# Kernel optimization log

Hardware: AMD Instinct MI355X
Metric: run time of the kernel (lower is better)

## Reference

```python
import jax, jax.numpy as jnp
import numpy as np

B, L, H = 2, 2048, 1024
NH, KVH = 16, 4
HD = H // NH          # 64
G = NH // KVH         # 4 query heads per kv head


def setup_inputs() -> dict:
    key = jax.random.key(0)
    ks = jax.random.split(key, 10)
    s = 0.02
    return {
        "hidden_states": jax.random.normal(ks[0], (B, L, H), dtype=jnp.float32),
        "attention_mask": jnp.zeros((B, 1, L, L), dtype=jnp.float32),
        "Wq": jax.random.normal(ks[1], (H, H), dtype=jnp.float32) * s,
        "bq": jnp.zeros((H,), dtype=jnp.float32),
        "Wk": jax.random.normal(ks[2], (KVH * HD, H), dtype=jnp.float32) * s,
        "bk": jnp.zeros((KVH * HD,), dtype=jnp.float32),
        "Wv": jax.random.normal(ks[3], (KVH * HD, H), dtype=jnp.float32) * s,
        "bv": jnp.zeros((KVH * HD,), dtype=jnp.float32),
        "Wo": jax.random.normal(ks[4], (H, H), dtype=jnp.float32) * s,
        "bo": jnp.zeros((H,), dtype=jnp.float32),
    }


def reference(hidden_states, attention_mask, Wq, bq, Wk, bk, Wv, bv, Wo, bo):
    x = hidden_states
    # projections (torch Linear: x @ W.T + b)
    q = (x @ Wq.T + bq).reshape(B, L, NH, HD).transpose(0, 2, 1, 3)   # [B,NH,L,HD]
    k = (x @ Wk.T + bk).reshape(B, L, KVH, HD).transpose(0, 2, 1, 3)  # [B,KVH,L,HD]
    v = (x @ Wv.T + bv).reshape(B, L, KVH, HD).transpose(0, 2, 1, 3)
    # GQA: group query heads per kv head instead of repeat_interleave (same math)
    qg = q.reshape(B, KVH, G, L, HD)
    scores = jnp.einsum("bkgqd,bkld->bkgql", qg, k) / jnp.sqrt(jnp.float32(HD))
    scores = scores + attention_mask[:, :, None, :, :]  # mask broadcasts over heads
    attn = jax.nn.softmax(scores, axis=-1)              # dropout p=0 -> identity
    ctx = jnp.einsum("bkgql,bkld->bkgqd", attn, v)      # [B,KVH,G,L,HD]
    ctx = ctx.reshape(B, NH, L, HD).transpose(0, 2, 1, 3).reshape(B, L, H)
    return ctx @ Wo.T + bo
```

## Files before the change

kernel.cpp:

```cpp
#include <hip/hip_runtime.h>

#define B_   2
#define L_   2048
#define H_   1024
#define NH_  16
#define KVH_ 4
#define HD_  64

typedef short short8 __attribute__((ext_vector_type(8)));
typedef float f32x4 __attribute__((ext_vector_type(4)));
typedef unsigned short u16x4 __attribute__((ext_vector_type(4)));
typedef unsigned int u32x2 __attribute__((ext_vector_type(2)));

#define LOG2E 1.4426950408889634f
#define QSC   0.18033688011112042f
#define MFMA  __builtin_amdgcn_mfma_f32_16x16x32_bf16

#if __has_builtin(__builtin_amdgcn_exp2f)
#define EXP2(x) __builtin_amdgcn_exp2f(x)
#else
#define EXP2(x) exp2f(x)
#endif

static __device__ __forceinline__ unsigned short f2bf(float f) {
  unsigned int u = __float_as_uint(f);
  u += 0x7FFFu + ((u >> 16) & 1u);
  return (unsigned short)(u >> 16);
}

static __device__ __forceinline__ unsigned int cvtpk(float lo, float hi) {
  unsigned int r;
  asm("v_cvt_pk_bf16_f32 %0, %1, %2" : "=v"(r) : "v"(lo), "v"(hi));
  return r;
}

static __device__ __forceinline__ void gload_lds16(const void* g, void* l) {
  __builtin_amdgcn_global_load_lds(
      (const __attribute__((address_space(1))) unsigned int*)g,
      (__attribute__((address_space(3))) unsigned int*)l, 16, 0, 0);
}

__global__ __launch_bounds__(256) void k_prep(const float* __restrict__ x,
                                              const float* __restrict__ Wq,
                                              const float* __restrict__ Wk,
                                              const float* __restrict__ Wv,
                                              const float* __restrict__ Wo,
                                              const float* __restrict__ mask,
                                              unsigned short* __restrict__ xb,
                                              unsigned short* __restrict__ wcat,
                                              unsigned short* __restrict__ wo_b,
                                              unsigned char* __restrict__ flags) {
  const int blk = blockIdx.x;
  const int t = threadIdx.x;
  if (blk < 4096) {
    size_t i = ((size_t)blk * 256 + t) * 4;
    float4 v = *(const float4*)(x + i);
    u16x4 o = { f2bf(v.x), f2bf(v.y), f2bf(v.z), f2bf(v.w) };
    *(u16x4*)(xb + i) = o;
  } else if (blk < 6656) {
    int r = blk - 4096;
    int c = t * 4;
    const float* src;
    unsigned short* dst;
    if (r < 1024)      { src = Wq + (size_t)r * 1024;          dst = wcat + (size_t)r * 1024; }
    else if (r < 1280) { src = Wk + (size_t)(r - 1024) * 1024; dst = wcat + (size_t)r * 1024; }
    else if (r < 1536) { src = Wv + (size_t)(r - 1280) * 1024; dst = wcat + (size_t)r * 1024; }
    else               { src = Wo + (size_t)(r - 1536) * 1024; dst = wo_b + (size_t)(r - 1536) * 1024; }
    float4 v = *(const float4*)(src + c);
    u16x4 o = { f2bf(v.x), f2bf(v.y), f2bf(v.z), f2bf(v.w) };
    *(u16x4*)(dst + c) = o;
  } else {
    const int mb = blk - 6656;
    const int b = mb >> 10, qb = (mb >> 5) & 31, kb = mb & 31;
    const float* base = mask + ((size_t)b * L_ + qb * 64) * L_ + kb * 64;
    const int r0 = t >> 4, c = (t & 15) * 4;
    bool nz = false;
#pragma unroll
    for (int i = 0; i < 4; ++i) {
      float4 v = *(const float4*)(base + (size_t)(r0 + i * 16) * L_ + c);
      nz |= (v.x != 0.f) | (v.y != 0.f) | (v.z != 0.f) | (v.w != 0.f);
    }
    __shared__ int anyv;
    if (t == 0) anyv = 0;
    __syncthreads();
    if (__any(nz) && (t & 63) == 0) atomicOr(&anyv, 1);
    __syncthreads();
    if (t == 0) flags[mb] = (unsigned char)anyv;
  }
}

template <int MODE>
__global__ __launch_bounds__(256) void k_gemm(const unsigned short* __restrict__ A,
                                              const unsigned short* __restrict__ Bt,
                                              const float* __restrict__ bias0,
                                              const float* __restrict__ bias1,
                                              const float* __restrict__ bias2,
                                              unsigned short* __restrict__ q_ws,
                                              unsigned short* __restrict__ k_ws,
                                              unsigned short* __restrict__ vt_ws,
                                              float* __restrict__ outp) {
  const int bn = blockIdx.x, bm = blockIdx.y;
  const int t = threadIdx.x;
  const int lane = t & 63, li = lane & 15, g = lane >> 4;
  const int wid = t >> 6, wr = wid >> 1, wc = wid & 1;
  __shared__ unsigned short lds_a[128 * 32];
  __shared__ unsigned short lds_b[128 * 32];

  const f32x4 z = {0.f, 0.f, 0.f, 0.f};
  f32x4 acc[4][4];
#pragma unroll
  for (int m = 0; m < 4; ++m)
#pragma unroll
    for (int n = 0; n < 4; ++n) acc[m][n] = z;

  const int c0 = t, c1 = 256 + t;
  const int r0 = c0 >> 2, o0 = (c0 & 3) * 8;
  const int r1 = c1 >> 2, o1 = (c1 & 3) * 8;
  const unsigned short* a0p = A + (size_t)(bm * 128 + r0) * 1024 + o0;
  const unsigned short* a1p = A + (size_t)(bm * 128 + r1) * 1024 + o1;
  const unsigned short* b0p = Bt + (size_t)(bn * 128 + r0) * 1024 + o0;
  const unsigned short* b1p = Bt + (size_t)(bn * 128 + r1) * 1024 + o1;

  for (int kt = 0; kt < 1024; kt += 32) {
    gload_lds16(a0p + kt, &lds_a[c0 * 8]);
    gload_lds16(a1p + kt, &lds_a[c1 * 8]);
    gload_lds16(b0p + kt, &lds_b[c0 * 8]);
    gload_lds16(b1p + kt, &lds_b[c1 * 8]);
    __syncthreads();
    short8 af[4], bf[4];
#pragma unroll
    for (int m = 0; m < 4; ++m) af[m] = *(const short8*)&lds_a[(wr * 64 + m * 16 + li) * 32 + g * 8];
#pragma unroll
    for (int n = 0; n < 4; ++n) bf[n] = *(const short8*)&lds_b[(wc * 64 + n * 16 + li) * 32 + g * 8];
#pragma unroll
    for (int m = 0; m < 4; ++m)
#pragma unroll
      for (int n = 0; n < 4; ++n)
        acc[m][n] = MFMA(af[m], bf[n], acc[m][n], 0, 0, 0);
    __syncthreads();
  }

#pragma unroll
  for (int m = 0; m < 4; ++m) {
    const int row0 = bm * 128 + wr * 64 + m * 16 + 4 * g;
#pragma unroll
    for (int n = 0; n < 4; ++n) {
      const int col = bn * 128 + wc * 64 + n * 16 + li;
      f32x4 v = acc[m][n];
      if (MODE == 1) {
        const float bias = bias0[col];
#pragma unroll
        for (int r = 0; r < 4; ++r) outp[(size_t)(row0 + r) * 1024 + col] = v[r] + bias;
      } else {
        if (col < 1024) {
          const float bias = bias0[col];
#pragma unroll
          for (int r = 0; r < 4; ++r) q_ws[(size_t)(row0 + r) * 1024 + col] = f2bf((v[r] + bias) * QSC);
        } else if (col < 1280) {
          const int cc = col - 1024;
          const float bias = bias1[cc];
#pragma unroll
          for (int r = 0; r < 4; ++r) k_ws[(size_t)(row0 + r) * 256 + cc] = f2bf(v[r] + bias);
        } else {
          const int cc = col - 1280;
          const float bias = bias2[cc];
          const int kvh = cc >> 6, d = cc & 63;
          const int b = row0 >> 11, l0 = row0 & 2047;
          u16x4 pk = { f2bf(v[0] + bias), f2bf(v[1] + bias), f2bf(v[2] + bias), f2bf(v[3] + bias) };
          *(u16x4*)(vt_ws + ((size_t)((b * KVH_ + kvh) * 64 + d)) * 2048 + l0) = pk;
        }
      }
    }
  }
}

__global__ __launch_bounds__(256, 2) void k_attn(const unsigned short* __restrict__ q_ws,
                                                 const unsigned short* __restrict__ k_ws,
                                                 const unsigned short* __restrict__ vt_ws,
                                                 const float* __restrict__ mask,
                                                 const unsigned char* __restrict__ mflags,
                                                 unsigned short* __restrict__ ctx) {
  const int bk = blockIdx.x;
  const int qt = blockIdx.y;
  const int b = bk >> 2, kvh = bk & 3;
  const int t = threadIdx.x;
  const int wid = t >> 6, lane = t & 63, li = lane & 15, g = lane >> 4;
  const int h = kvh * 4 + wid;

  __shared__ unsigned short lds_k[3][64 * 64];
  __shared__ unsigned short lds_v[3][64 * 64];
  __shared__ unsigned short lds_p[4][2][16 * 72];

  const unsigned short* qlane = q_ws + ((size_t)b * L_ + qt * 32 + li) * H_ + h * HD_ + g * 8;
  short8 qf[2][2];
#pragma unroll
  for (int qif = 0; qif < 2; ++qif)
#pragma unroll
    for (int hh = 0; hh < 2; ++hh)
      qf[qif][hh] = *(const short8*)(qlane + (size_t)qif * 16 * H_ + hh * 32);

  const unsigned int* fp = (const unsigned int*)(mflags + b * 1024 + (qt >> 1) * 32);
  unsigned int fm = 0;
#pragma unroll
  for (int w = 0; w < 8; ++w) {
    unsigned int wv = fp[w];
    fm |= ((wv & 0x000000FFu) ? 1u : 0u) << (w * 4 + 0);
    fm |= ((wv & 0x0000FF00u) ? 1u : 0u) << (w * 4 + 1);
    fm |= ((wv & 0x00FF0000u) ? 1u : 0u) << (w * 4 + 2);
    fm |= ((wv & 0xFF000000u) ? 1u : 0u) << (w * 4 + 3);
  }
  fm = __builtin_amdgcn_readfirstlane(fm);

  const int srow = t >> 3, sgr = t & 7;
  const int swz = (sgr ^ (srow & 7)) * 8;
  const unsigned short* ksrc = k_ws + ((size_t)b * L_ + srow) * 256 + kvh * 64 + swz;
  const unsigned short* vsrc = vt_ws + ((size_t)(b * KVH_ + kvh) * 64 + srow) * 2048 + swz;

  const f32x4 z = {0.f, 0.f, 0.f, 0.f};
  f32x4 o[2][4];
#pragma unroll
  for (int qif = 0; qif < 2; ++qif)
#pragma unroll
    for (int db = 0; db < 4; ++db) o[qif][db] = z;
  float l_run[2] = {0.f, 0.f};

  const int rsw = li & 7;

#define STAGE(buf, kt)                                                       \
  {                                                                          \
    _Pragma("unroll")                                                        \
    for (int i = 0; i < 2; ++i) {                                            \
      gload_lds16(ksrc + ((size_t)(kt) * 64 + i * 32) * 256,                 \
                  &lds_k[buf][(t + 256 * i) * 8]);                           \
      gload_lds16(vsrc + (size_t)i * 32 * 2048 + (kt) * 64,                  \
                  &lds_v[buf][(t + 256 * i) * 8]);                           \
    }                                                                        \
  }

  auto readK = [&](short8 (&kf)[4][2], int buf) {
#pragma unroll
    for (int x = 0; x < 4; ++x) {
      const int row = (x * 16 + li) * 64;
      kf[x][0] = *(const short8*)&lds_k[buf][row + ((0 + g) ^ rsw) * 8];
      kf[x][1] = *(const short8*)&lds_k[buf][row + ((4 + g) ^ rsw) * 8];
    }
  };

  auto tile = [&](short8 (&kfc)[4][2], short8 (&kfn)[4][2], int kt) {
    const int cur = kt % 3;
    if (kt + 2 < 32) STAGE((kt + 2) % 3, kt + 2);

    short8 vf[4][2];
#pragma unroll
    for (int x = 0; x < 4; ++x) {
      const int row = (x * 16 + li) * 64;
      vf[x][0] = *(const short8*)&lds_v[cur][row + ((0 + g) ^ rsw) * 8];
      vf[x][1] = *(const short8*)&lds_v[cur][row + ((4 + g) ^ rsw) * 8];
    }

    f32x4 sv[2][4];
    __builtin_amdgcn_s_setprio(1);
#pragma unroll
    for (int qif = 0; qif < 2; ++qif)
#pragma unroll
      for (int kb = 0; kb < 4; ++kb) {
        sv[qif][kb] = MFMA(kfc[kb][0], qf[qif][0], z, 0, 0, 0);
        sv[qif][kb] = MFMA(kfc[kb][1], qf[qif][1], sv[qif][kb], 0, 0, 0);
      }
    __builtin_amdgcn_s_setprio(0);

    if (kt + 1 < 32) readK(kfn, (kt + 1) % 3);

    if (fm & (1u << kt)) {
#pragma unroll
      for (int qif = 0; qif < 2; ++qif) {
        const float* mrow = mask + ((size_t)b * L_ + qt * 32 + qif * 16 + li) * L_ + kt * 64 + 4 * g;
#pragma unroll
        for (int kb = 0; kb < 4; ++kb) {
          float4 mv = *(const float4*)(mrow + kb * 16);
          sv[qif][kb][0] = fmaf(mv.x, LOG2E, sv[qif][kb][0]);
          sv[qif][kb][1] = fmaf(mv.y, LOG2E, sv[qif][kb][1]);
          sv[qif][kb][2] = fmaf(mv.z, LOG2E, sv[qif][kb][2]);
          sv[qif][kb][3] = fmaf(mv.w, LOG2E, sv[qif][kb][3]);
        }
      }
    }

#pragma unroll
    for (int qif = 0; qif < 2; ++qif) {
      float ts = 0.f;
#pragma unroll
      for (int kb = 0; kb < 4; ++kb)
#pragma unroll
        for (int r = 0; r < 4; ++r) {
          const float p = EXP2(sv[qif][kb][r]);
          sv[qif][kb][r] = p;
          ts += p;
        }
      l_run[qif] += ts;
#pragma unroll
      for (int kb = 0; kb < 4; ++kb) {
        u32x2 pk = { cvtpk(sv[qif][kb][0], sv[qif][kb][1]),
                     cvtpk(sv[qif][kb][2], sv[qif][kb][3]) };
        *(u32x2*)&lds_p[wid][qif][li * 72 + kb * 16 + 4 * g] = pk;
      }
    }

    __builtin_amdgcn_s_setprio(1);
#pragma unroll
    for (int qif = 0; qif < 2; ++qif)
#pragma unroll
      for (int kjh = 0; kjh < 2; ++kjh) {
        short8 pb = *(const short8*)&lds_p[wid][qif][li * 72 + kjh * 32 + g * 8];
#pragma unroll
        for (int db = 0; db < 4; ++db)
          o[qif][db] = MFMA(vf[db][kjh], pb, o[qif][db], 0, 0, 0);
      }
    __builtin_amdgcn_s_setprio(0);

    __syncthreads();
  };

  STAGE(0, 0);
  __syncthreads();
  STAGE(1, 1);
  __syncthreads();

  short8 kfA[4][2], kfB[4][2];
  readK(kfA, 0);

#pragma unroll 1
  for (int kt = 0; kt < 32; kt += 2) {
    tile(kfA, kfB, kt);
    tile(kfB, kfA, kt + 1);
  }
#undef STAGE

#pragma unroll
  for (int qif = 0; qif < 2; ++qif) {
    float lt = l_run[qif];
    lt += __shfl_xor(lt, 16);
    lt += __shfl_xor(lt, 32);
    const float inv = 1.0f / lt;
    unsigned short* cp = ctx + ((size_t)b * L_ + qt * 32 + qif * 16 + li) * H_ + h * HD_ + 4 * g;
#pragma unroll
    for (int db = 0; db < 4; ++db) {
      u32x2 pk = { cvtpk(o[qif][db][0] * inv, o[qif][db][1] * inv),
                   cvtpk(o[qif][db][2] * inv, o[qif][db][3] * inv) };
      *(u32x2*)(cp + db * 16) = pk;
    }
  }
}

extern "C" void kernel_launch(void* const* d_in, const int* in_sizes, int n_in,
                              void* d_out, int out_size, void* d_ws, size_t ws_size,
                              hipStream_t stream) {
  const float* x    = (const float*)d_in[0];
  const float* mask = (const float*)d_in[1];
  const float* Wq   = (const float*)d_in[2];
  const float* bq   = (const float*)d_in[3];
  const float* Wk   = (const float*)d_in[4];
  const float* bk   = (const float*)d_in[5];
  const float* Wv   = (const float*)d_in[6];
  const float* bv   = (const float*)d_in[7];
  const float* Wo   = (const float*)d_in[8];
  const float* bo   = (const float*)d_in[9];
  float* out = (float*)d_out;

  char* ws = (char*)d_ws;
  unsigned short* xb    = (unsigned short*)(ws);
  unsigned short* ctx   = xb;
  unsigned short* wcat  = (unsigned short*)(ws + 8388608);
  unsigned short* wo_b  = (unsigned short*)(ws + 11534336);
  unsigned short* q_ws  = (unsigned short*)(ws + 13631488);
  unsigned short* k_ws  = (unsigned short*)(ws + 22020096);
  unsigned short* vt_ws = (unsigned short*)(ws + 24117248);
  unsigned char*  mflg  = (unsigned char*)(ws + 26214400);

  k_prep<<<dim3(8704), dim3(256), 0, stream>>>(x, Wq, Wk, Wv, Wo, mask, xb, wcat, wo_b, mflg);
  k_gemm<0><<<dim3(12, 32), dim3(256), 0, stream>>>(xb, wcat, bq, bk, bv, q_ws, k_ws, vt_ws, nullptr);
  k_attn<<<dim3(8, 64), dim3(256), 0, stream>>>(q_ws, k_ws, vt_ws, mask, mflg, ctx);
  k_gemm<1><<<dim3(8, 32), dim3(256), 0, stream>>>(ctx, wo_b, bo, nullptr, nullptr,
                                                   nullptr, nullptr, nullptr, out);
}
```

Measured before the change: 116.5 us.

## Restructure attention with 32x32 MFMA, register P via permlane swap, split-K waves

The attention kernel switches from 16x16x32 to 32x32x16 bf16 MFMA. Each wave now handles two query heads over half of the key tile, with partial outputs and row sums combined through LDS at the end. The probability tile is moved into the PV operand layout with v_permlane32_swap instead of an LDS round trip, and K/V staging drops from triple to double buffering. The aim is to cut LDS traffic and instruction count per tile, at the cost of a final cross-wave reduction and less prefetch depth.

```diff
diff --git a/kernel.cpp b/kernel.cpp
--- a/kernel.cpp
+++ b/kernel.cpp
@@ -9,12 +9,13 @@
 
 typedef short short8 __attribute__((ext_vector_type(8)));
 typedef float f32x4 __attribute__((ext_vector_type(4)));
+typedef float f32x16 __attribute__((ext_vector_type(16)));
 typedef unsigned short u16x4 __attribute__((ext_vector_type(4)));
-typedef unsigned int u32x2 __attribute__((ext_vector_type(2)));
 
 #define LOG2E 1.4426950408889634f
 #define QSC   0.18033688011112042f
-#define MFMA  __builtin_amdgcn_mfma_f32_16x16x32_bf16
+#define MFMA   __builtin_amdgcn_mfma_f32_16x16x32_bf16
+#define MFMA32 __builtin_amdgcn_mfma_f32_32x32x16_bf16
 
 #if __has_builtin(__builtin_amdgcn_exp2f)
 #define EXP2(x) __builtin_amdgcn_exp2f(x)
@@ -32,6 +33,17 @@
   unsigned int r;
   asm("v_cvt_pk_bf16_f32 %0, %1, %2" : "=v"(r) : "v"(lo), "v"(hi));
   return r;
+}
+
+static __device__ __forceinline__ void plswap(unsigned int& a, unsigned int& b) {
+  asm("v_permlane32_swap_b32 %0, %1" : "+v"(a), "+v"(b));
+}
+
+static __device__ __forceinline__ short8 mk8(unsigned int w0, unsigned int w1,
+                                             unsigned int w2, unsigned int w3) {
+  union { unsigned int u[4]; short8 s; } x;
+  x.u[0] = w0; x.u[1] = w1; x.u[2] = w2; x.u[3] = w3;
+  return x.s;
 }
 
 static __device__ __forceinline__ void gload_lds16(const void* g, void* l) {
@@ -184,20 +196,21 @@
   const int qt = blockIdx.y;
   const int b = bk >> 2, kvh = bk & 3;
   const int t = threadIdx.x;
-  const int wid = t >> 6, lane = t & 63, li = lane & 15, g = lane >> 4;
-  const int h = kvh * 4 + wid;
-
-  __shared__ unsigned short lds_k[3][64 * 64];
-  __shared__ unsigned short lds_v[3][64 * 64];
-  __shared__ unsigned short lds_p[4][2][16 * 72];
-
-  const unsigned short* qlane = q_ws + ((size_t)b * L_ + qt * 32 + li) * H_ + h * HD_ + g * 8;
-  short8 qf[2][2];
-#pragma unroll
-  for (int qif = 0; qif < 2; ++qif)
-#pragma unroll
-    for (int hh = 0; hh < 2; ++hh)
-      qf[qif][hh] = *(const short8*)(qlane + (size_t)qif * 16 * H_ + hh * 32);
+  const int wid = t >> 6, lane = t & 63;
+  const int l31 = lane & 31, g1 = lane >> 5;
+  const int kh = wid >> 1, hp = wid & 1;
+
+  __shared__ unsigned short smem[16384];
+  __shared__ float lred[2][2][64];
+
+  const unsigned short* qbase = q_ws + ((size_t)b * L_ + qt * 32 + l31) * H_ +
+                                (kvh * 4 + hp * 2) * 64 + g1 * 8;
+  short8 qf[2][4];
+#pragma unroll
+  for (int h2 = 0; h2 < 2; ++h2)
+#pragma unroll
+    for (int ks = 0; ks < 4; ++ks)
+      qf[h2][ks] = *(const short8*)(qbase + h2 * 64 + ks * 16);
 
   const unsigned int* fp = (const unsigned int*)(mflags + b * 1024 + (qt >> 1) * 32);
   unsigned int fm = 0;
@@ -216,138 +229,178 @@
   const unsigned short* ksrc = k_ws + ((size_t)b * L_ + srow) * 256 + kvh * 64 + swz;
   const unsigned short* vsrc = vt_ws + ((size_t)(b * KVH_ + kvh) * 64 + srow) * 2048 + swz;
 
-  const f32x4 z = {0.f, 0.f, 0.f, 0.f};
-  f32x4 o[2][4];
-#pragma unroll
-  for (int qif = 0; qif < 2; ++qif)
-#pragma unroll
-    for (int db = 0; db < 4; ++db) o[qif][db] = z;
-  float l_run[2] = {0.f, 0.f};
-
-  const int rsw = li & 7;
-
-#define STAGE(buf, kt)                                                       \
-  {                                                                          \
-    _Pragma("unroll")                                                        \
-    for (int i = 0; i < 2; ++i) {                                            \
-      gload_lds16(ksrc + ((size_t)(kt) * 64 + i * 32) * 256,                 \
-                  &lds_k[buf][(t + 256 * i) * 8]);                           \
-      gload_lds16(vsrc + (size_t)i * 32 * 2048 + (kt) * 64,                  \
-                  &lds_v[buf][(t + 256 * i) * 8]);                           \
-    }                                                                        \
-  }
-
-  auto readK = [&](short8 (&kf)[4][2], int buf) {
-#pragma unroll
-    for (int x = 0; x < 4; ++x) {
-      const int row = (x * 16 + li) * 64;
-      kf[x][0] = *(const short8*)&lds_k[buf][row + ((0 + g) ^ rsw) * 8];
-      kf[x][1] = *(const short8*)&lds_k[buf][row + ((4 + g) ^ rsw) * 8];
-    }
-  };
-
-  auto tile = [&](short8 (&kfc)[4][2], short8 (&kfn)[4][2], int kt) {
-    const int cur = kt % 3;
-    if (kt + 2 < 32) STAGE((kt + 2) % 3, kt + 2);
-
-    short8 vf[4][2];
-#pragma unroll
-    for (int x = 0; x < 4; ++x) {
-      const int row = (x * 16 + li) * 64;
-      vf[x][0] = *(const short8*)&lds_v[cur][row + ((0 + g) ^ rsw) * 8];
-      vf[x][1] = *(const short8*)&lds_v[cur][row + ((4 + g) ^ rsw) * 8];
-    }
-
-    f32x4 sv[2][4];
-    __builtin_amdgcn_s_setprio(1);
-#pragma unroll
-    for (int qif = 0; qif < 2; ++qif)
-#pragma unroll
-      for (int kb = 0; kb < 4; ++kb) {
-        sv[qif][kb] = MFMA(kfc[kb][0], qf[qif][0], z, 0, 0, 0);
-        sv[qif][kb] = MFMA(kfc[kb][1], qf[qif][1], sv[qif][kb], 0, 0, 0);
-      }
-    __builtin_amdgcn_s_setprio(0);
-
-    if (kt + 1 < 32) readK(kfn, (kt + 1) % 3);
-
-    if (fm & (1u << kt)) {
-#pragma unroll
-      for (int qif = 0; qif < 2; ++qif) {
-        const float* mrow = mask + ((size_t)b * L_ + qt * 32 + qif * 16 + li) * L_ + kt * 64 + 4 * g;
-#pragma unroll
-        for (int kb = 0; kb < 4; ++kb) {
-          float4 mv = *(const float4*)(mrow + kb * 16);
-          sv[qif][kb][0] = fmaf(mv.x, LOG2E, sv[qif][kb][0]);
-          sv[qif][kb][1] = fmaf(mv.y, LOG2E, sv[qif][kb][1]);
-          sv[qif][kb][2] = fmaf(mv.z, LOG2E, sv[qif][kb][2]);
-          sv[qif][kb][3] = fmaf(mv.w, LOG2E, sv[qif][kb][3]);
-        }
-      }
-    }
-
-#pragma unroll
-    for (int qif = 0; qif < 2; ++qif) {
-      float ts = 0.f;
-#pragma unroll
-      for (int kb = 0; kb < 4; ++kb)
-#pragma unroll
-        for (int r = 0; r < 4; ++r) {
-          const float p = EXP2(sv[qif][kb][r]);
-          sv[qif][kb][r] = p;
-          ts += p;
-        }
-      l_run[qif] += ts;
-#pragma unroll
-      for (int kb = 0; kb < 4; ++kb) {
-        u32x2 pk = { cvtpk(sv[qif][kb][0], sv[qif][kb][1]),
-                     cvtpk(sv[qif][kb][2], sv[qif][kb][3]) };
-        *(u32x2*)&lds_p[wid][qif][li * 72 + kb * 16 + 4 * g] = pk;
-      }
-    }
-
-    __builtin_amdgcn_s_setprio(1);
-#pragma unroll
-    for (int qif = 0; qif < 2; ++qif)
-#pragma unroll
-      for (int kjh = 0; kjh < 2; ++kjh) {
-        short8 pb = *(const short8*)&lds_p[wid][qif][li * 72 + kjh * 32 + g * 8];
-#pragma unroll
-        for (int db = 0; db < 4; ++db)
-          o[qif][db] = MFMA(vf[db][kjh], pb, o[qif][db], 0, 0, 0);
-      }
-    __builtin_amdgcn_s_setprio(0);
-
-    __syncthreads();
-  };
+  f32x16 o_[4];
+  const f32x16 z16 = {0,0,0,0,0,0,0,0,0,0,0,0,0,0,0,0};
+#pragma unroll
+  for (int i = 0; i < 4; ++i) o_[i] = z16;
+  float l_part[2] = {0.f, 0.f};
+
+  const int rK = kh * 32 + l31, swK = rK & 7;
+  const int rV0 = l31, rV1 = 32 + l31;
+  const int swV0 = rV0 & 7, swV1 = rV1 & 7;
+
+#define STAGE(buf, kt)                                                        \
+  {                                                                           \
+    unsigned short* dk = smem + (buf) * 8192;                                 \
+    unsigned short* dv = dk + 4096;                                           \
+    _Pragma("unroll")                                                         \
+    for (int i = 0; i < 2; ++i) {                                             \
+      gload_lds16(ksrc + ((size_t)(kt) * 64 + i * 32) * 256, dk + (t + 256 * i) * 8); \
+      gload_lds16(vsrc + (size_t)i * 32 * 2048 + (kt) * 64,  dv + (t + 256 * i) * 8); \
+    }                                                                         \
+  }
 
   STAGE(0, 0);
   __syncthreads();
-  STAGE(1, 1);
+
+#pragma unroll 1
+  for (int kt = 0; kt < 32; ++kt) {
+    const int cur = kt & 1;
+    if (kt + 1 < 32) STAGE(cur ^ 1, kt + 1);
+
+    const unsigned short* lk = smem + cur * 8192;
+    const unsigned short* lv = lk + 4096;
+
+    short8 kf[4];
+#pragma unroll
+    for (int ks = 0; ks < 4; ++ks)
+      kf[ks] = *(const short8*)&lk[rK * 64 + ((ks * 2 + g1) ^ swK) * 8];
+    short8 vf[2][2];
+#pragma unroll
+    for (int s = 0; s < 2; ++s) {
+      vf[0][s] = *(const short8*)&lv[rV0 * 64 + ((kh * 4 + s * 2 + g1) ^ swV0) * 8];
+      vf[1][s] = *(const short8*)&lv[rV1 * 64 + ((kh * 4 + s * 2 + g1) ^ swV1) * 8];
+    }
+
+    f32x16 sv[2];
+    sv[0] = z16; sv[1] = z16;
+    __builtin_amdgcn_s_setprio(1);
+#pragma unroll
+    for (int ks = 0; ks < 4; ++ks) sv[0] = MFMA32(kf[ks], qf[0][ks], sv[0], 0, 0, 0);
+#pragma unroll
+    for (int ks = 0; ks < 4; ++ks) sv[1] = MFMA32(kf[ks], qf[1][ks], sv[1], 0, 0, 0);
+    __builtin_amdgcn_s_setprio(0);
+
+    if (fm & (1u << kt)) {
+      const float* mrow = mask + ((size_t)b * L_ + qt * 32 + l31) * L_ + kt * 64 + kh * 32 + g1 * 4;
+#pragma unroll
+      for (int rg = 0; rg < 4; ++rg) {
+        float4 mv = *(const float4*)(mrow + rg * 8);
+#pragma unroll
+        for (int j = 0; j < 4; ++j) {
+          const float mj = (&mv.x)[j] * LOG2E;
+          sv[0][rg * 4 + j] += mj;
+          sv[1][rg * 4 + j] += mj;
+        }
+      }
+    }
+
+    short8 pa[2][2];
+#pragma unroll
+    for (int h2 = 0; h2 < 2; ++h2) {
+      float e[16];
+#pragma unroll
+      for (int r = 0; r < 16; ++r) e[r] = EXP2(sv[h2][r]);
+      l_part[h2] += (((e[0] + e[1]) + (e[2] + e[3])) + ((e[4] + e[5]) + (e[6] + e[7]))) +
+                    (((e[8] + e[9]) + (e[10] + e[11])) + ((e[12] + e[13]) + (e[14] + e[15])));
+      unsigned int w0 = cvtpk(e[0], e[1]),   w1 = cvtpk(e[2], e[3]);
+      unsigned int w2 = cvtpk(e[4], e[5]),   w3 = cvtpk(e[6], e[7]);
+      unsigned int w4 = cvtpk(e[8], e[9]),   w5 = cvtpk(e[10], e[11]);
+      unsigned int w6 = cvtpk(e[12], e[13]), w7 = cvtpk(e[14], e[15]);
+      plswap(w0, w2); plswap(w1, w3);
+      plswap(w4, w6); plswap(w5, w7);
+      pa[h2][0] = mk8(w0, w1, w2, w3);
+      pa[h2][1] = mk8(w4, w5, w6, w7);
+    }
+
+    __builtin_amdgcn_s_setprio(1);
+#pragma unroll
+    for (int h2 = 0; h2 < 2; ++h2)
+#pragma unroll
+      for (int db = 0; db < 2; ++db) {
+        o_[h2 * 2 + db] = MFMA32(vf[db][0], pa[h2][0], o_[h2 * 2 + db], 0, 0, 0);
+        o_[h2 * 2 + db] = MFMA32(vf[db][1], pa[h2][1], o_[h2 * 2 + db], 0, 0, 0);
+      }
+    __builtin_amdgcn_s_setprio(0);
+
+    __syncthreads();
+  }
+#undef STAGE
+
+  float lt0 = l_part[0] + __shfl_xor(l_part[0], 32);
+  float lt1 = l_part[1] + __shfl_xor(l_part[1], 32);
+  float* red = (float*)smem;
+
+  if (kh == 1) {
+    lred[hp][0][lane] = lt0;
+    lred[hp][1][lane] = lt1;
+#pragma unroll
+    for (int db = 0; db < 2; ++db)
+#pragma unroll
+      for (int w4 = 0; w4 < 4; ++w4) {
+        f32x4 pv = { o_[db][w4 * 4 + 0], o_[db][w4 * 4 + 1],
+                     o_[db][w4 * 4 + 2], o_[db][w4 * 4 + 3] };
+        *(f32x4*)&red[(((w4 * 2 + hp) * 2 + db) * 64 + lane) * 4] = pv;
+      }
+  }
   __syncthreads();
 
-  short8 kfA[4][2], kfB[4][2];
-  readK(kfA, 0);
-
-#pragma unroll 1
-  for (int kt = 0; kt < 32; kt += 2) {
-    tile(kfA, kfB, kt);
-    tile(kfB, kfA, kt + 1);
-  }
-#undef STAGE
-
-#pragma unroll
-  for (int qif = 0; qif < 2; ++qif) {
-    float lt = l_run[qif];
-    lt += __shfl_xor(lt, 16);
-    lt += __shfl_xor(lt, 32);
-    const float inv = 1.0f / lt;
-    unsigned short* cp = ctx + ((size_t)b * L_ + qt * 32 + qif * 16 + li) * H_ + h * HD_ + 4 * g;
-#pragma unroll
-    for (int db = 0; db < 4; ++db) {
-      u32x2 pk = { cvtpk(o[qif][db][0] * inv, o[qif][db][1] * inv),
-                   cvtpk(o[qif][db][2] * inv, o[qif][db][3] * inv) };
-      *(u32x2*)(cp + db * 16) = pk;
+  if (kh == 0) {
+    const float inv = 1.f / (lt0 + lred[hp][0][lane]);
+#pragma unroll
+    for (int db = 0; db < 2; ++db) {
+      f32x16 acc = o_[db];
+#pragma unroll
+      for (int w4 = 0; w4 < 4; ++w4) {
+        f32x4 pv = *(const f32x4*)&red[(((w4 * 2 + hp) * 2 + db) * 64 + lane) * 4];
+#pragma unroll
+        for (int j = 0; j < 4; ++j) acc[w4 * 4 + j] += pv[j];
+      }
+      unsigned short* cp = ctx + ((size_t)b * L_ + qt * 32 + l31) * H_ +
+                           (kvh * 4 + hp * 2) * 64 + db * 32 + g1 * 4;
+#pragma unroll
+      for (int k4 = 0; k4 < 4; ++k4) {
+        unsigned int a0 = cvtpk(acc[4 * k4 + 0] * inv, acc[4 * k4 + 1] * inv);
+        unsigned int a1 = cvtpk(acc[4 * k4 + 2] * inv, acc[4 * k4 + 3] * inv);
+        *(unsigned int*)(cp + 8 * k4) = a0;
+        *(unsigned int*)(cp + 8 * k4 + 2) = a1;
+      }
+    }
+  }
+  __syncthreads();
+
+  if (kh == 1) {
+#pragma unroll
+    for (int db = 0; db < 2; ++db)
+#pragma unroll
+      for (int w4 = 0; w4 < 4; ++w4) {
+        f32x4 pv = { o_[2 + db][w4 * 4 + 0], o_[2 + db][w4 * 4 + 1],
+                     o_[2 + db][w4 * 4 + 2], o_[2 + db][w4 * 4 + 3] };
+        *(f32x4*)&red[(((w4 * 2 + hp) * 2 + db) * 64 + lane) * 4] = pv;
+      }
+  }
+  __syncthreads();
+
+  if (kh == 0) {
+    const float inv = 1.f / (lt1 + lred[hp][1][lane]);
+#pragma unroll
+    for (int db = 0; db < 2; ++db) {
+      f32x16 acc = o_[2 + db];
+#pragma unroll
+      for (int w4 = 0; w4 < 4; ++w4) {
+        f32x4 pv = *(const f32x4*)&red[(((w4 * 2 + hp) * 2 + db) * 64 + lane) * 4];
+#pragma unroll
+        for (int j = 0; j < 4; ++j) acc[w4 * 4 + j] += pv[j];
+      }
+      unsigned short* cp = ctx + ((size_t)b * L_ + qt * 32 + l31) * H_ +
+                           (kvh * 4 + hp * 2 + 1) * 64 + db * 32 + g1 * 4;
+#pragma unroll
+      for (int k4 = 0; k4 < 4; ++k4) {
+        unsigned int a0 = cvtpk(acc[4 * k4 + 0] * inv, acc[4 * k4 + 1] * inv);
+        unsigned int a1 = cvtpk(acc[4 * k4 + 2] * inv, acc[4 * k4 + 3] * inv);
+        *(unsigned int*)(cp + 8 * k4) = a0;
+        *(unsigned int*)(cp + 8 * k4 + 2) = a1;
+      }
     }
   }
 }
```

After: 114.1 us. 2.1% less time.
